# Kernel tuning notes

Measured on AMD Instinct MI355X. Metric: run time of the kernel, lower is better.

## Reference

```python
import jax, jax.numpy as jnp
import numpy as np

N, W, T = 8, 64, 8192      # batch, emb_width, time
K_BINS = 2048

def setup_inputs() -> dict:
    key = jax.random.key(0)
    kx, kk = jax.random.split(key)
    x = jax.random.normal(kx, (N, W, T), dtype=jnp.float32)
    k = jax.random.normal(kk, (K_BINS, W), dtype=jnp.float32)
    return {"x": x, "k": k}

def reference(x, k):
    n, w, t = x.shape
    # preprocess: (N, W, T) -> (N*T, W)
    xf = jnp.transpose(x, (0, 2, 1)).reshape(-1, w)
    prenorm = jnp.linalg.norm(xf - jnp.mean(xf)) / np.sqrt(float(xf.size))
    # quantise: squared-euclidean distances via matmul expansion
    # dist[i, j] = ||xf_i||^2 - 2 xf_i . k_j + ||k_j||^2   -> (N*T, K_BINS)
    dist = (jnp.sum(xf * xf, axis=-1, keepdims=True)
            - 2.0 * (xf @ k.T)
            + jnp.sum(k * k, axis=-1)[None, :])
    x_l = jnp.argmin(dist, axis=-1)            # (N*T,)
    fit = jnp.mean(jnp.min(dist, axis=-1))
    # dequantise: embedding gather
    x_d = k[x_l]                               # (N*T, W)
    commit_loss = jnp.sum((jax.lax.stop_gradient(x_d) - xf) ** 2) / float(xf.size)
    # straight-through estimator
    x_d = xf + jax.lax.stop_gradient(x_d - xf)
    # postprocess
    x_l = x_l.reshape(n, t)
    x_d = jnp.transpose(x_d.reshape(n, t, w), (0, 2, 1))  # (N, W, T)
    return x_l, x_d, commit_loss, fit, prenorm
```

## Files before the change

kernel.cpp:

```cpp
#include <hip/hip_runtime.h>
#include <hip/hip_bf16.h>
#include <math.h>

#define N_BATCH 8
#define WDIM 64
#define TDIM 8192
#define KBINS 2048
#define NROWS (N_BATCH * TDIM)
#define XSIZE (N_BATCH * WDIM * TDIM)
#define XL_OFF 0
#define XD_OFF NROWS
#define SCAL_OFF (NROWS + XSIZE)

#define MT 64
#define XST 72
#define TAU 0.05f
#define MAXFLAG 8192
#define NBLK (NROWS / MT)

#define WS_K2_OFF   0
#define WS_CNT_OFF  8192
#define WS_FLAG_OFF 8256
#define WS_SLOT_OFF 41024
#define WS_PART_OFF 106560
#define WS_KF_OFF   122944
#define WS_KT_OFF   647296
#define WS_KT_END   (WS_KT_OFF + (size_t)WDIM * KBINS * 4)
#define WS_XF_OFF   WS_KT_END
#define WS_XF_END   (WS_XF_OFF + (size_t)MAXFLAG * WDIM * 4)

typedef __attribute__((ext_vector_type(8))) short bf16x8;
typedef __attribute__((ext_vector_type(4))) float f32x4;
typedef unsigned long long u64;

static __device__ __forceinline__ short f2bf(float v) {
  __hip_bfloat16 b = __float2bfloat16(v);
  return *reinterpret_cast<short*>(&b);
}
static __device__ __forceinline__ float bf2f(short s) {
  unsigned int u = ((unsigned int)(unsigned short)s) << 16;
  return __uint_as_float(u);
}

#define GLOAD_LDS(gsrc, ldst)                                            \
  __builtin_amdgcn_global_load_lds(                                      \
      (const __attribute__((address_space(1))) unsigned int*)(gsrc),     \
      (__attribute__((address_space(3))) unsigned int*)(ldst), 16, 0, 0)

#define WAIT_VM4 0x0F74
#define WAIT_VM0 0x0F70
#define SBAR() asm volatile("s_barrier" ::: "memory")

__global__ void prep_kernel(const float* __restrict__ kg, float* __restrict__ k2,
                            char* __restrict__ kfrag, float* __restrict__ kT,
                            int* __restrict__ cnt, u64* __restrict__ slots) {
  __shared__ float skc[16 * 65];
  const int tid  = threadIdx.x;
  const int tile = blockIdx.x;
  const int c0   = tile * 16;
  if (tile == 0 && tid == 0) *cnt = 0;
  if (tid < 64) slots[tile * 64 + tid] = ~0ULL;
  {
    const float4* g4 = (const float4*)(kg + (size_t)c0 * WDIM);
    int code = tid >> 4, w = (tid & 15) * 4;
    *(float4*)&skc[code * 65 + w] = g4[tid];
  }
  __syncthreads();
  if (tid < 16) {
    const float* kr = &skc[tid * 65];
    float r[8];
#pragma unroll
    for (int l = 0; l < 8; ++l) r[l] = __fmul_rn(kr[l], kr[l]);
    for (int i = 8; i < WDIM; i += 8) {
#pragma unroll
      for (int l = 0; l < 8; ++l)
        r[l] = __fadd_rn(r[l], __fmul_rn(kr[i + l], kr[i + l]));
    }
    k2[c0 + tid] = __fadd_rn(__fadd_rn(__fadd_rn(r[0], r[1]), __fadd_rn(r[2], r[3])),
                             __fadd_rn(__fadd_rn(r[4], r[5]), __fadd_rn(r[6], r[7])));
  }
  if (kT) {
    const int code = tid & 15;
#pragma unroll
    for (int j = 0; j < 4; ++j) {
      int w = (tid >> 4) + 16 * j;
      kT[(size_t)w * KBINS + c0 + code] = skc[code * 65 + w];
    }
  }
  {
    const int sub  = tid >> 6;
    const int lane = tid & 63;
    const int lcol = lane & 15;
    const int quad = lane >> 4;
    const float* src = &skc[lcol * 65 + (sub & 1) * 32 + quad * 8];
    const bool lo = (sub >= 2);
    short tmp[8];
#pragma unroll
    for (int i = 0; i < 8; ++i) {
      float v = src[i];
      short h = f2bf(v);
      tmp[i] = lo ? f2bf(v - bf2f(h)) : h;
    }
    char* dst = kfrag + (size_t)tile * 4096 + sub * 1024 + lane * 16;
    *(bf16x8*)dst = *(const bf16x8*)tmp;
  }
}

__launch_bounds__(256, 4)
__global__ void vq_mono(const float* __restrict__ x,
                        const float* __restrict__ kg,
                        const float* __restrict__ k2g,
                        const char* __restrict__ kfrag,
                        float* __restrict__ out,
                        float* __restrict__ part,
                        int* __restrict__ flag_cnt,
                        int* __restrict__ flags,
                        float* __restrict__ xf) {
  __shared__ __align__(16) char smem[20480];
  char*  kbuf = smem;
  float* k2f  = (float*)(smem + 12288);
  short* sxh = (short*)smem;
  short* sxl = (short*)(smem + 9216);
  float* kd  = (float*)smem;
  int*   sIdx      = (int*)  (smem + 18432);
  float* sPair     = (float*)(smem + 18688);
  int*   sFlagCnt  = (int*)  (smem + 18752);
  int*   sFlagBase = (int*)  (smem + 18756);
  int*   sFlagList = (int*)  (smem + 18760);

  const int tid  = threadIdx.x;
  const int blk  = blockIdx.x;
  const int row0 = blk * MT;
  const int n    = row0 >> 13;
  const int t0   = row0 & (TDIM - 1);

  const int r  = tid & 63;
  const int wh = tid >> 6;
  float x2p = 0.f, sxp = 0.f;
  const float* xb = x + (size_t)n * WDIM * TDIM + t0 + r;
#pragma unroll 8
  for (int i = 0; i < 16; ++i) {
    int w = 4 * i + wh;
    float v = xb[(size_t)w * TDIM];
    x2p = fmaf(v, v, x2p);
    sxp += v;
    short h = f2bf(v);
    sxh[r * XST + w] = h;
    sxl[r * XST + w] = f2bf(v - bf2f(h));
  }
  __syncthreads();

  const int wave = tid >> 6;
  const int lane = tid & 63;
  const int lcol = lane & 15;
  const int quad = lane >> 4;
  const int rA = wave * 16 + lcol;
  bf16x8 ah0 = *(const bf16x8*)&sxh[rA * XST + 0  + quad * 8];
  bf16x8 ah1 = *(const bf16x8*)&sxh[rA * XST + 32 + quad * 8];
  bf16x8 al0 = *(const bf16x8*)&sxl[rA * XST + 0  + quad * 8];
  bf16x8 al1 = *(const bf16x8*)&sxl[rA * XST + 32 + quad * 8];
  __syncthreads();

  float bd[4], b2[4];
  int   bi[4];
#pragma unroll
  for (int i = 0; i < 4; ++i) { bd[i] = 3.0e38f; b2[i] = 3.0e38f; bi[i] = 0; }

  const char* kfg = kfrag;

#define VQM_ISSUE(C, B)                                                      \
  if ((C) < 128) {                                                           \
    const char* s = kfg + (size_t)(C) * 4096 + (lane << 4);                  \
    char* d = kbuf + (B) * 4096;                                             \
    GLOAD_LDS(s, d);                                                         \
    GLOAD_LDS(s + 1024, d + 1024);                                           \
    GLOAD_LDS(s + 2048, d + 2048);                                           \
    GLOAD_LDS(s + 3072, d + 3072);                                           \
  }

  {
    const float4* k24 = (const float4*)k2g;
    *(float4*)&k2f[tid * 8]     = k24[tid * 2];
    *(float4*)&k2f[tid * 8 + 4] = k24[tid * 2 + 1];
  }
  if (wave == 0) {
    VQM_ISSUE(0, 0)
    VQM_ISSUE(1, 1)
  }
  asm volatile("s_waitcnt lgkmcnt(0)\n\ts_barrier" ::: "memory");

#define VQM_STEP(C, RB, PB, WAITIMM)                                         \
  {                                                                          \
    if (wave == 0) __builtin_amdgcn_s_waitcnt(WAITIMM);                      \
    SBAR();                                                                  \
    const char* tb = kbuf + (RB) * 4096;                                     \
    bf16x8 bh0 = *(const bf16x8*)(tb + 0    + (lane << 4));                  \
    bf16x8 bh1 = *(const bf16x8*)(tb + 1024 + (lane << 4));                  \
    bf16x8 bl0 = *(const bf16x8*)(tb + 2048 + (lane << 4));                  \
    bf16x8 bl1 = *(const bf16x8*)(tb + 3072 + (lane << 4));                  \
    float k2c = k2f[(C) * 16 + lcol];                                        \
    if (wave == 0) { VQM_ISSUE((C) + 2, PB) }                                \
    f32x4 p = {0.f, 0.f, 0.f, 0.f};                                          \
    p = __builtin_amdgcn_mfma_f32_16x16x32_bf16(ah0, bh0, p, 0, 0, 0);       \
    p = __builtin_amdgcn_mfma_f32_16x16x32_bf16(ah1, bh1, p, 0, 0, 0);       \
    p = __builtin_amdgcn_mfma_f32_16x16x32_bf16(ah0, bl0, p, 0, 0, 0);       \
    p = __builtin_amdgcn_mfma_f32_16x16x32_bf16(ah1, bl1, p, 0, 0, 0);       \
    p = __builtin_amdgcn_mfma_f32_16x16x32_bf16(al0, bh0, p, 0, 0, 0);       \
    p = __builtin_amdgcn_mfma_f32_16x16x32_bf16(al1, bh1, p, 0, 0, 0);       \
    const int code = (C) * 16 + lcol;                                        \
    _Pragma("unroll")                                                        \
    for (int i = 0; i < 4; ++i) {                                            \
      float d0 = fmaf(-2.f, p[i], k2c);                                      \
      float nb2 = __builtin_amdgcn_fmed3f(bd[i], d0, b2[i]);                 \
      bool lt0 = d0 < bd[i];                                                 \
      bd[i] = lt0 ? d0 : bd[i];                                              \
      bi[i] = lt0 ? code : bi[i];                                            \
      b2[i] = nb2;                                                           \
    }                                                                        \
  }

  for (int c = 0; c < 126; c += 3) {
    VQM_STEP(c,     0, 2, WAIT_VM4)
    VQM_STEP(c + 1, 1, 0, WAIT_VM4)
    VQM_STEP(c + 2, 2, 1, WAIT_VM4)
  }
  VQM_STEP(126, 0, 2, WAIT_VM4)
  VQM_STEP(127, 1, 0, WAIT_VM0)
#undef VQM_STEP
#undef VQM_ISSUE

#pragma unroll
  for (int m = 1; m < 16; m <<= 1) {
#pragma unroll
    for (int i = 0; i < 4; ++i) {
      float od  = __shfl_xor(bd[i], m, 64);
      float od2 = __shfl_xor(b2[i], m, 64);
      int   oi  = __shfl_xor(bi[i], m, 64);
      float nb2 = fminf(fminf(b2[i], od2), fmaxf(bd[i], od));
      bool take = (od < bd[i]) || (od == bd[i] && oi < bi[i]);
      bd[i] = take ? od : bd[i];
      bi[i] = take ? oi : bi[i];
      b2[i] = nb2;
    }
  }

  __syncthreads();
  if (tid == 0) *sFlagCnt = 0;
  __syncthreads();

  float fit_p = 0.f;
  if (lcol == 0) {
#pragma unroll
    for (int i = 0; i < 4; ++i) {
      int rloc = wave * 16 + quad * 4 + i;
      int rowg = row0 + rloc;
      out[XL_OFF + rowg] = (float)bi[i];
      sIdx[rloc] = bi[i];
      fit_p += bd[i];
      if (b2[i] - bd[i] < TAU) {
        int slot = atomicAdd(sFlagCnt, 1);
        sFlagList[slot] = rowg;
      }
    }
  }
  __syncthreads();

  int nloc = *sFlagCnt;
  if (tid == 0 && nloc > 0) *sFlagBase = atomicAdd(flag_cnt, nloc);
  __syncthreads();
  if (tid < nloc) {
    int gs = *sFlagBase + tid;
    if (gs < MAXFLAG) flags[gs] = sFlagList[tid];
  }

  if (xf) {
    for (int i = 0; i < nloc; ++i) {
      int gs = *sFlagBase + i;
      if (gs >= MAXFLAG) break;
      int rloc = sFlagList[i] - row0;
      if (r == rloc) {
#pragma unroll
        for (int ii = 0; ii < 16; ++ii)
          xf[(size_t)gs * WDIM + 4 * ii + wh] = xb[(size_t)(4 * ii + wh) * TDIM];
      }
    }
  }

  {
    int rr = tid >> 2, q4 = tid & 3;
    const float4* kr4 = (const float4*)(kg + (size_t)sIdx[rr] * WDIM) + q4 * 4;
    float4* dst = (float4*)&kd[rr * 68 + q4 * 16];
#pragma unroll
    for (int j = 0; j < 4; ++j) dst[j] = kr4[j];
  }
  __syncthreads();

  float commit_p = 0.f;
  float* xdb = out + XD_OFF + (size_t)n * WDIM * TDIM + t0 + r;
#pragma unroll 8
  for (int i = 0; i < 16; ++i) {
    int w = 4 * i + wh;
    float xvv = xb[(size_t)w * TDIM];
    float kvv = kd[r * 68 + w];
    float df = kvv - xvv;
    commit_p = fmaf(df, df, commit_p);
    xdb[(size_t)w * TDIM] = kvv;
  }

  float v0 = sxp, v1 = x2p, v2 = commit_p, v3 = fit_p;
#pragma unroll
  for (int off = 32; off > 0; off >>= 1) {
    v0 += __shfl_down(v0, off, 64);
    v1 += __shfl_down(v1, off, 64);
    v2 += __shfl_down(v2, off, 64);
    v3 += __shfl_down(v3, off, 64);
  }
  if (lane == 0) {
    sPair[wave * 4 + 0] = v0;
    sPair[wave * 4 + 1] = v1;
    sPair[wave * 4 + 2] = v2;
    sPair[wave * 4 + 3] = v3;
  }
  __syncthreads();
  if (tid == 0) {
    float x2sum = sPair[1] + sPair[5] + sPair[9] + sPair[13];
    part[0 * NBLK + blk] = sPair[0] + sPair[4] + sPair[8] + sPair[12];
    part[1 * NBLK + blk] = x2sum;
    part[2 * NBLK + blk] = sPair[2] + sPair[6] + sPair[10] + sPair[14];
    part[3 * NBLK + blk] = (sPair[3] + sPair[7] + sPair[11] + sPair[15]) + x2sum;
  }
}

__launch_bounds__(256, 2)
__global__ void recheck_scan(const float* __restrict__ x,
                             const float* __restrict__ xf,
                             const float* __restrict__ kg,
                             const float* __restrict__ kT,
                             const float* __restrict__ k2g,
                             const int* __restrict__ flag_cnt,
                             const int* __restrict__ flags,
                             u64* __restrict__ slots) {
  __shared__ float sx[WDIM];
  __shared__ float sx2s;
  __shared__ u64 swm[4];
  const int tid  = threadIdx.x;
  const int lane = tid & 63;
  const int wv   = tid >> 6;
  int nf = *flag_cnt;
  if (nf > MAXFLAG) nf = MAXFLAG;

  for (int fi = blockIdx.x; fi < nf; fi += 2048) {
    const int row = flags[fi];
    if (tid < WDIM) {
      if (xf) {
        sx[tid] = xf[(size_t)fi * WDIM + tid];
      } else {
        int n = row >> 13, t = row & (TDIM - 1);
        sx[tid] = x[(size_t)n * WDIM * TDIM + (size_t)tid * TDIM + t];
      }
    }
    __syncthreads();
    if (tid == 0) {
      float r8[8];
#pragma unroll
      for (int l = 0; l < 8; ++l) r8[l] = __fmul_rn(sx[l], sx[l]);
      for (int i = 8; i < WDIM; i += 8) {
#pragma unroll
        for (int l = 0; l < 8; ++l)
          r8[l] = __fadd_rn(r8[l], __fmul_rn(sx[i + l], sx[i + l]));
      }
      sx2s = __fadd_rn(__fadd_rn(__fadd_rn(r8[0], r8[1]), __fadd_rn(r8[2], r8[3])),
                       __fadd_rn(__fadd_rn(r8[4], r8[5]), __fadd_rn(r8[6], r8[7])));
    }
    __syncthreads();

    float xreg[WDIM];
#pragma unroll
    for (int w = 0; w < WDIM; ++w) xreg[w] = sx[w];
    const float sx2v = sx2s;

    u64 best = ~0ULL;
#pragma unroll 1
    for (int s = 0; s < 4; ++s) {
      const int j0 = s * 256 + tid;
      const int j1 = j0 + 1024;
      float c0 = 0.f, c1 = 0.f;
      if (kT) {
#pragma unroll
        for (int w = 0; w < WDIM; ++w) {
          c0 = __fmaf_rn(xreg[w], kT[(size_t)w * KBINS + j0], c0);
          c1 = __fmaf_rn(xreg[w], kT[(size_t)w * KBINS + j1], c1);
        }
      } else {
        const float* kr0 = kg + (size_t)j0 * WDIM;
        const float* kr1 = kg + (size_t)j1 * WDIM;
#pragma unroll
        for (int w = 0; w < WDIM; ++w) {
          c0 = __fmaf_rn(xreg[w], kr0[w], c0);
          c1 = __fmaf_rn(xreg[w], kr1[w], c1);
        }
      }
      float d0 = __fadd_rn(__fsub_rn(sx2v, __fmul_rn(2.0f, c0)), k2g[j0]);
      float d1 = __fadd_rn(__fsub_rn(sx2v, __fmul_rn(2.0f, c1)), k2g[j1]);
      u64 key0 = ((u64)__float_as_uint(d0) << 32) | (unsigned)j0;
      u64 key1 = ((u64)__float_as_uint(d1) << 32) | (unsigned)j1;
      if (key0 < best) best = key0;
      if (key1 < best) best = key1;
    }
#pragma unroll
    for (int off = 32; off > 0; off >>= 1) {
      u64 o = __shfl_down((unsigned long long)best, off, 64);
      if (o < best) best = o;
    }
    if (lane == 0) swm[wv] = best;
    __syncthreads();
    if (tid == 0) {
      u64 b = swm[0];
#pragma unroll
      for (int k = 1; k < 4; ++k) b = (swm[k] < b) ? swm[k] : b;
      atomicMin(&slots[fi], b);
    }
    __syncthreads();
  }
}

__global__ void recheck_write(const float* __restrict__ kg,
                              const int* __restrict__ flag_cnt,
                              const int* __restrict__ flags,
                              const u64* __restrict__ slots,
                              float* __restrict__ out) {
  int nf = *flag_cnt;
  if (nf > MAXFLAG) nf = MAXFLAG;
  const int w = threadIdx.x;
  for (int fi = blockIdx.x; fi < nf; fi += 256) {
    const int row = flags[fi];
    const int n = row >> 13;
    const int t = row & (TDIM - 1);
    const int j = (int)(slots[fi] & 0xFFFFFFFFULL);
    if (w == 0) out[XL_OFF + row] = (float)j;
    out[XD_OFF + (size_t)n * WDIM * TDIM + (size_t)w * TDIM + t] = kg[(size_t)j * WDIM + w];
  }
}

__global__ void finalize_kernel(const float* __restrict__ part, float* __restrict__ out) {
  __shared__ double sred[4][64];
  const int tid = threadIdx.x;
  const int lane = tid & 63;
  const int wv = tid >> 6;
  double a[4] = {0.0, 0.0, 0.0, 0.0};
  for (int i = tid; i < NBLK; i += 256) {
#pragma unroll
    for (int q = 0; q < 4; ++q) a[q] += (double)part[q * NBLK + i];
  }
#pragma unroll
  for (int off = 32; off > 0; off >>= 1) {
#pragma unroll
    for (int q = 0; q < 4; ++q)
      a[q] += __shfl_down(a[q], off, 64);
  }
  if (lane == 0) {
#pragma unroll
    for (int q = 0; q < 4; ++q) sred[q][wv] = a[q];
  }
  __syncthreads();
  if (tid == 0) {
    double s0 = 0, s1 = 0, s2 = 0, s3 = 0;
#pragma unroll
    for (int wv2 = 0; wv2 < 4; ++wv2) {
      s0 += sred[0][wv2]; s1 += sred[1][wv2];
      s2 += sred[2][wv2]; s3 += sred[3][wv2];
    }
    double size = (double)XSIZE;
    double commit = s2 / size;
    double fit = s3 / (double)NROWS;
    double mean = s0 / size;
    double var = s1 / size - mean * mean;
    if (var < 0.0) var = 0.0;
    out[SCAL_OFF + 0] = (float)commit;
    out[SCAL_OFF + 1] = (float)fit;
    out[SCAL_OFF + 2] = (float)sqrt(var);
  }
}

extern "C" void kernel_launch(void* const* d_in, const int* in_sizes, int n_in,
                              void* d_out, int out_size, void* d_ws, size_t ws_size,
                              hipStream_t stream) {
  const float* x = (const float*)d_in[0];
  const float* kg = (const float*)d_in[1];
  float* out = (float*)d_out;
  float* k2   = (float*)((char*)d_ws + WS_K2_OFF);
  int* cnt    = (int*)((char*)d_ws + WS_CNT_OFF);
  int* flags  = (int*)((char*)d_ws + WS_FLAG_OFF);
  u64* slots  = (u64*)((char*)d_ws + WS_SLOT_OFF);
  float* part = (float*)((char*)d_ws + WS_PART_OFF);
  char* kfrag = (char*)d_ws + WS_KF_OFF;
  float* kT   = (ws_size >= WS_KT_END) ? (float*)((char*)d_ws + WS_KT_OFF) : nullptr;
  float* xf   = (ws_size >= WS_XF_END) ? (float*)((char*)d_ws + WS_XF_OFF) : nullptr;

  hipLaunchKernelGGL(prep_kernel, dim3(KBINS / 16), dim3(256), 0, stream,
                     kg, k2, kfrag, kT, cnt, slots);
  hipLaunchKernelGGL(vq_mono, dim3(NBLK), dim3(256), 0, stream,
                     x, kg, k2, kfrag, out, part, cnt, flags, xf);
  hipLaunchKernelGGL(recheck_scan, dim3(2048), dim3(256), 0, stream,
                     x, xf, kg, kT, k2, cnt, flags, slots);
  hipLaunchKernelGGL(recheck_write, dim3(256), dim3(WDIM), 0, stream,
                     kg, cnt, flags, slots, out);
  hipLaunchKernelGGL(finalize_kernel, dim3(1), dim3(256), 0, stream, part, out);
}
```

Baseline: 173.9 us.

## Batch flagged-row recheck across 64 rows per block with codebook held in registers

The fp32 recheck kernel used to process one flagged row per block and reread the full codebook for every row. It now processes batches of 64 flagged rows, each block owning a 256-code chunk kept in registers, and reads the rows transposed from LDS, so each codebook load is reused across 64 rows. The argmin is reduced per wave with a shuffle-min plus ballot for the lowest index, then merged across waves and blocks with atomicMin. Separately, the main kernel now writes flagged rows' x values into the scratch buffer inside the existing commit loop, replacing a serial per-flag loop. The cost is 64 codebook values held in registers per thread and a launch sized for the maximum flag count, where most blocks exit early.

```diff
diff --git a/kernel.cpp b/kernel.cpp
--- a/kernel.cpp
+++ b/kernel.cpp
@@ -17,6 +17,7 @@
 #define TAU 0.05f
 #define MAXFLAG 8192
 #define NBLK (NROWS / MT)
+#define RB 64
 
 #define WS_K2_OFF   0
 #define WS_CNT_OFF  8192
@@ -127,6 +128,7 @@
   int*   sFlagCnt  = (int*)  (smem + 18752);
   int*   sFlagBase = (int*)  (smem + 18756);
   int*   sFlagList = (int*)  (smem + 18760);
+  int*   rowSlot   = (int*)  (smem + 19016);
 
   const int tid  = threadIdx.x;
   const int blk  = blockIdx.x;
@@ -189,11 +191,11 @@
   }
   asm volatile("s_waitcnt lgkmcnt(0)\n\ts_barrier" ::: "memory");
 
-#define VQM_STEP(C, RB, PB, WAITIMM)                                         \
+#define VQM_STEP(C, RB_, PB, WAITIMM)                                        \
   {                                                                          \
     if (wave == 0) __builtin_amdgcn_s_waitcnt(WAITIMM);                      \
     SBAR();                                                                  \
-    const char* tb = kbuf + (RB) * 4096;                                     \
+    const char* tb = kbuf + (RB_) * 4096;                                    \
     bf16x8 bh0 = *(const bf16x8*)(tb + 0    + (lane << 4));                  \
     bf16x8 bh1 = *(const bf16x8*)(tb + 1024 + (lane << 4));                  \
     bf16x8 bl0 = *(const bf16x8*)(tb + 2048 + (lane << 4));                  \
@@ -246,6 +248,7 @@
 
   __syncthreads();
   if (tid == 0) *sFlagCnt = 0;
+  if (tid < MT) rowSlot[tid] = -1;
   __syncthreads();
 
   float fit_p = 0.f;
@@ -270,19 +273,9 @@
   __syncthreads();
   if (tid < nloc) {
     int gs = *sFlagBase + tid;
-    if (gs < MAXFLAG) flags[gs] = sFlagList[tid];
-  }
-
-  if (xf) {
-    for (int i = 0; i < nloc; ++i) {
-      int gs = *sFlagBase + i;
-      if (gs >= MAXFLAG) break;
-      int rloc = sFlagList[i] - row0;
-      if (r == rloc) {
-#pragma unroll
-        for (int ii = 0; ii < 16; ++ii)
-          xf[(size_t)gs * WDIM + 4 * ii + wh] = xb[(size_t)(4 * ii + wh) * TDIM];
-      }
+    if (gs < MAXFLAG) {
+      flags[gs] = sFlagList[tid];
+      rowSlot[sFlagList[tid] - row0] = gs;
     }
   }
 
@@ -296,6 +289,7 @@
   __syncthreads();
 
   float commit_p = 0.f;
+  const int sl = xf ? rowSlot[r] : -1;
   float* xdb = out + XD_OFF + (size_t)n * WDIM * TDIM + t0 + r;
 #pragma unroll 8
   for (int i = 0; i < 16; ++i) {
@@ -305,6 +299,7 @@
     float df = kvv - xvv;
     commit_p = fmaf(df, df, commit_p);
     xdb[(size_t)w * TDIM] = kvv;
+    if (sl >= 0) xf[(size_t)sl * WDIM + w] = xvv;
   }
 
   float v0 = sxp, v1 = x2p, v2 = commit_p, v3 = fit_p;
@@ -340,87 +335,118 @@
                              const int* __restrict__ flag_cnt,
                              const int* __restrict__ flags,
                              u64* __restrict__ slots) {
-  __shared__ float sx[WDIM];
-  __shared__ float sx2s;
-  __shared__ u64 swm[4];
+  __shared__ __align__(16) float xrT[WDIM * 72];
+  __shared__ float sx2r[RB];
+  __shared__ u64   wkey[RB][4];
+  __shared__ int   rowsA[RB];
   const int tid  = threadIdx.x;
   const int lane = tid & 63;
   const int wv   = tid >> 6;
   int nf = *flag_cnt;
   if (nf > MAXFLAG) nf = MAXFLAG;
-
-  for (int fi = blockIdx.x; fi < nf; fi += 2048) {
-    const int row = flags[fi];
-    if (tid < WDIM) {
-      if (xf) {
-        sx[tid] = xf[(size_t)fi * WDIM + tid];
-      } else {
+  const int batch = blockIdx.x >> 3;
+  const int chunk = blockIdx.x & 7;
+  const int f0 = batch * RB;
+  if (f0 >= nf) return;
+  const int nr = min(RB, nf - f0);
+
+  if (xf) {
+    const float* src = xf + (size_t)f0 * WDIM;
+#pragma unroll
+    for (int i = 0; i < 16; ++i) {
+      int idx = tid + i * 256;
+      int rr = idx >> 6, w = idx & 63;
+      float v = (rr < nr) ? src[idx] : 0.f;
+      xrT[w * 72 + rr] = v;
+    }
+  } else {
+    if (tid < RB) rowsA[tid] = (tid < nr) ? flags[f0 + tid] : 0;
+    __syncthreads();
+#pragma unroll
+    for (int i = 0; i < 16; ++i) {
+      int idx = tid + i * 256;
+      int rr = idx >> 6, w = idx & 63;
+      float v = 0.f;
+      if (rr < nr) {
+        int row = rowsA[rr];
         int n = row >> 13, t = row & (TDIM - 1);
-        sx[tid] = x[(size_t)n * WDIM * TDIM + (size_t)tid * TDIM + t];
+        v = x[(size_t)n * WDIM * TDIM + (size_t)w * TDIM + t];
       }
-    }
-    __syncthreads();
-    if (tid == 0) {
-      float r8[8];
-#pragma unroll
-      for (int l = 0; l < 8; ++l) r8[l] = __fmul_rn(sx[l], sx[l]);
-      for (int i = 8; i < WDIM; i += 8) {
-#pragma unroll
-        for (int l = 0; l < 8; ++l)
-          r8[l] = __fadd_rn(r8[l], __fmul_rn(sx[i + l], sx[i + l]));
+      xrT[w * 72 + rr] = v;
+    }
+  }
+  __syncthreads();
+
+  if (tid < RB) {
+    float r8[8];
+#pragma unroll
+    for (int l = 0; l < 8; ++l) {
+      float vv = xrT[l * 72 + tid];
+      r8[l] = __fmul_rn(vv, vv);
+    }
+    for (int i = 8; i < WDIM; i += 8) {
+#pragma unroll
+      for (int l = 0; l < 8; ++l) {
+        float vv = xrT[(i + l) * 72 + tid];
+        r8[l] = __fadd_rn(r8[l], __fmul_rn(vv, vv));
       }
-      sx2s = __fadd_rn(__fadd_rn(__fadd_rn(r8[0], r8[1]), __fadd_rn(r8[2], r8[3])),
-                       __fadd_rn(__fadd_rn(r8[4], r8[5]), __fadd_rn(r8[6], r8[7])));
-    }
-    __syncthreads();
-
-    float xreg[WDIM];
-#pragma unroll
-    for (int w = 0; w < WDIM; ++w) xreg[w] = sx[w];
-    const float sx2v = sx2s;
-
-    u64 best = ~0ULL;
+    }
+    sx2r[tid] = __fadd_rn(__fadd_rn(__fadd_rn(r8[0], r8[1]), __fadd_rn(r8[2], r8[3])),
+                          __fadd_rn(__fadd_rn(r8[4], r8[5]), __fadd_rn(r8[6], r8[7])));
+  }
+  __syncthreads();
+
+  const int j = chunk * 256 + tid;
+  float kreg[WDIM];
+  if (kT) {
+#pragma unroll
+    for (int w = 0; w < WDIM; ++w) kreg[w] = kT[(size_t)w * KBINS + j];
+  } else {
+    const float* kr = kg + (size_t)j * WDIM;
+#pragma unroll
+    for (int w = 0; w < WDIM; ++w) kreg[w] = kr[w];
+  }
+  const float k2j = k2g[j];
+
 #pragma unroll 1
-    for (int s = 0; s < 4; ++s) {
-      const int j0 = s * 256 + tid;
-      const int j1 = j0 + 1024;
-      float c0 = 0.f, c1 = 0.f;
-      if (kT) {
-#pragma unroll
-        for (int w = 0; w < WDIM; ++w) {
-          c0 = __fmaf_rn(xreg[w], kT[(size_t)w * KBINS + j0], c0);
-          c1 = __fmaf_rn(xreg[w], kT[(size_t)w * KBINS + j1], c1);
-        }
-      } else {
-        const float* kr0 = kg + (size_t)j0 * WDIM;
-        const float* kr1 = kg + (size_t)j1 * WDIM;
-#pragma unroll
-        for (int w = 0; w < WDIM; ++w) {
-          c0 = __fmaf_rn(xreg[w], kr0[w], c0);
-          c1 = __fmaf_rn(xreg[w], kr1[w], c1);
-        }
-      }
-      float d0 = __fadd_rn(__fsub_rn(sx2v, __fmul_rn(2.0f, c0)), k2g[j0]);
-      float d1 = __fadd_rn(__fsub_rn(sx2v, __fmul_rn(2.0f, c1)), k2g[j1]);
-      u64 key0 = ((u64)__float_as_uint(d0) << 32) | (unsigned)j0;
-      u64 key1 = ((u64)__float_as_uint(d1) << 32) | (unsigned)j1;
-      if (key0 < best) best = key0;
-      if (key1 < best) best = key1;
-    }
-#pragma unroll
-    for (int off = 32; off > 0; off >>= 1) {
-      u64 o = __shfl_down((unsigned long long)best, off, 64);
-      if (o < best) best = o;
-    }
-    if (lane == 0) swm[wv] = best;
-    __syncthreads();
-    if (tid == 0) {
-      u64 b = swm[0];
-#pragma unroll
-      for (int k = 1; k < 4; ++k) b = (swm[k] < b) ? swm[k] : b;
-      atomicMin(&slots[fi], b);
-    }
-    __syncthreads();
+  for (int rg = 0; rg < 8; ++rg) {
+    float acc[8];
+#pragma unroll
+    for (int t8 = 0; t8 < 8; ++t8) acc[t8] = 0.f;
+#pragma unroll
+    for (int w = 0; w < WDIM; ++w) {
+      float4 xa = *(const float4*)&xrT[w * 72 + rg * 8];
+      float4 xb4 = *(const float4*)&xrT[w * 72 + rg * 8 + 4];
+      acc[0] = __fmaf_rn(xa.x, kreg[w], acc[0]);
+      acc[1] = __fmaf_rn(xa.y, kreg[w], acc[1]);
+      acc[2] = __fmaf_rn(xa.z, kreg[w], acc[2]);
+      acc[3] = __fmaf_rn(xa.w, kreg[w], acc[3]);
+      acc[4] = __fmaf_rn(xb4.x, kreg[w], acc[4]);
+      acc[5] = __fmaf_rn(xb4.y, kreg[w], acc[5]);
+      acc[6] = __fmaf_rn(xb4.z, kreg[w], acc[6]);
+      acc[7] = __fmaf_rn(xb4.w, kreg[w], acc[7]);
+    }
+#pragma unroll
+    for (int t8 = 0; t8 < 8; ++t8) {
+      const int rr = rg * 8 + t8;
+      float d = __fadd_rn(__fsub_rn(sx2r[rr], __fmul_rn(2.0f, acc[t8])), k2j);
+      float dmin = d;
+#pragma unroll
+      for (int m = 1; m < 64; m <<= 1)
+        dmin = fminf(dmin, __shfl_xor(dmin, m, 64));
+      u64 mask = __ballot(d == dmin);
+      int lowlane = __ffsll(mask) - 1;
+      u64 key = ((u64)__float_as_uint(dmin) << 32)
+              | (unsigned)(chunk * 256 + wv * 64 + lowlane);
+      if (lane == 0) wkey[rr][wv] = key;
+    }
+  }
+  __syncthreads();
+  if (tid < nr) {
+    u64 b = wkey[tid][0];
+#pragma unroll
+    for (int k = 1; k < 4; ++k) b = (wkey[tid][k] < b) ? wkey[tid][k] : b;
+    atomicMin(&slots[f0 + tid], b);
   }
 }
 
@@ -501,7 +527,7 @@
                      kg, k2, kfrag, kT, cnt, slots);
   hipLaunchKernelGGL(vq_mono, dim3(NBLK), dim3(256), 0, stream,
                      x, kg, k2, kfrag, out, part, cnt, flags, xf);
-  hipLaunchKernelGGL(recheck_scan, dim3(2048), dim3(256), 0, stream,
+  hipLaunchKernelGGL(recheck_scan, dim3((MAXFLAG / RB) * 8), dim3(256), 0, stream,
                      x, xf, kg, kT, k2, cnt, flags, slots);
   hipLaunchKernelGGL(recheck_write, dim3(256), dim3(WDIM), 0, stream,
                      kg, cnt, flags, slots, out);
```

After: 539.0 us. 3.1x slower.
